# Kernel tuning notes

Hardware: AMD Instinct MI355X
Metric: run time of the kernel (lower is better)

The kernel has to match this reference:

```python
import jax, jax.numpy as jnp
from jax import lax
import numpy as np

SPATIAL_IMPORTANCE = 1.0


def _ssn(x, nspix, n_iter):
    # x: [B, C, H, W]; SLIC-style soft superpixel clustering.
    B, C, H, W = x.shape
    g = int(round(nspix ** 0.5))  # grid side (16 for nspix=256)
    bh, bw = H // g, W // g
    pix = x.reshape(B, C, H * W)                      # [B, C, N]
    # grid initialization of superpixel centers: block-average pooling
    centers = x.reshape(B, C, g, bh, g, bw).mean(axis=(3, 5)).reshape(B, C, nspix)
    p2 = jnp.sum(pix * pix, axis=1)                   # [B, N]

    def affinity(centers):
        c2 = jnp.sum(centers * centers, axis=1)       # [B, K]
        dot = jnp.einsum('bcn,bck->bnk', pix, centers)
        dist = p2[:, :, None] + c2[:, None, :] - 2.0 * dot  # [B, N, K]
        return jax.nn.softmax(-dist, axis=-1)         # soft assignment [B, N, K]

    def step(centers, _):
        aff = affinity(centers)
        wsum = jnp.sum(aff, axis=1)                   # [B, K]
        new_c = jnp.einsum('bcn,bnk->bck', pix, aff) / (wsum[:, None, :] + 1e-16)
        return new_c, None

    centers, _ = lax.scan(step, centers, None, length=n_iter)
    aff = affinity(centers)                           # final soft assignment
    return jnp.transpose(aff, (0, 2, 1))              # [B, K, N]


def setup_inputs() -> dict:
    key = jax.random.key(0)
    x = jax.random.normal(key, (2, 5, 512, 512), dtype=jnp.float32)
    return {"x": x, "nspix": 256, "n_iter": 10}


def reference(x, nspix, n_iter):
    C = x.shape[1]
    scale = jnp.ones((C,), dtype=x.dtype).at[0].set(SPATIAL_IMPORTANCE).at[1].set(SPATIAL_IMPORTANCE)
    x = x * scale[None, :, None, None]
    return _ssn(x, nspix, n_iter)
```

## Files before the change

kernel.cpp:

```cpp
#include <hip/hip_runtime.h>
#include <hip/hip_bf16.h>


#define B_ 2
#define C_ 5
#define H_ 512
#define W_ 512
#define N_ (H_*W_)
#define K_ 256
#define NITER_ 10
#define T_ 512
#define LOG2E 1.4426950408889634f

typedef float f32x8 __attribute__((ext_vector_type(8)));
typedef float f32x4 __attribute__((ext_vector_type(4)));

__global__ __launch_bounds__(256) void init_centers(const float* __restrict__ x,
                                                    float* __restrict__ ctab) {
    int bk  = blockIdx.x;
    int b   = bk >> 8;
    int k   = bk & (K_ - 1);
    int gy  = k >> 4, gx = k & 15;
    int tid = threadIdx.x;

    float s[C_] = {0.f, 0.f, 0.f, 0.f, 0.f};
    for (int i = tid; i < 1024; i += 256) {
        int py = i >> 5, px = i & 31;
        int n  = (gy * 32 + py) * W_ + gx * 32 + px;
        const float* xb = x + (size_t)b * C_ * N_ + n;
        #pragma unroll
        for (int c = 0; c < C_; c++) s[c] += xb[(size_t)c * N_];
    }
    #pragma unroll
    for (int c = 0; c < C_; c++) {
        #pragma unroll
        for (int off = 32; off > 0; off >>= 1)
            s[c] += __shfl_down(s[c], off, 64);
    }
    __shared__ float wred[4][C_];
    int lane = tid & 63, wid = tid >> 6;
    if (lane == 0) {
        #pragma unroll
        for (int c = 0; c < C_; c++) wred[wid][c] = s[c];
    }
    __syncthreads();
    if (tid == 0) {
        float m[C_]; float c2 = 0.f;
        #pragma unroll
        for (int c = 0; c < C_; c++) {
            m[c] = (wred[0][c] + wred[1][c] + wred[2][c] + wred[3][c]) * (1.0f / 1024.0f);
            c2  += m[c] * m[c];
        }
        float* row = ctab + (size_t)(b * K_ + k) * 8;
        #pragma unroll
        for (int c = 0; c < C_; c++) row[c] = 2.0f * LOG2E * m[c];
        row[5] = -LOG2E * c2;
        row[6] = 0.f; row[7] = 0.f;
    }
}

__global__ __launch_bounds__(256, 4) void step_kernel(const float* __restrict__ x,
                                                      const float* __restrict__ ctab,
                                                      float* __restrict__ acc) {
    __shared__ float pl[C_][T_];
    __shared__ float rs[T_];
    int bid = blockIdx.x;
    int b   = bid >> 9;
    int n0  = (bid & 511) * T_;
    int tid = threadIdx.x;

    const float* xb = x + (size_t)b * C_ * N_ + n0;
    #pragma unroll
    for (int c = 0; c < C_; c++) {
        pl[c][tid]       = xb[(size_t)c * N_ + tid];
        pl[c][tid + 256] = xb[(size_t)c * N_ + tid + 256];
    }
    __syncthreads();

    float p0[C_], p1[C_];
    #pragma unroll
    for (int c = 0; c < C_; c++) { p0[c] = pl[c][tid]; p1[c] = pl[c][tid + 256]; }

    const f32x8* crow = (const f32x8*)(ctab + (size_t)b * K_ * 8);
    float S0 = 0.f, S1 = 0.f;
    #pragma unroll 8
    for (int k = 0; k < K_; k++) {
        f32x8 r = crow[k];
        float l0 = r[5], l1 = r[5];
        l0 = fmaf(r[0], p0[0], l0);  l1 = fmaf(r[0], p1[0], l1);
        l0 = fmaf(r[1], p0[1], l0);  l1 = fmaf(r[1], p1[1], l1);
        l0 = fmaf(r[2], p0[2], l0);  l1 = fmaf(r[2], p1[2], l1);
        l0 = fmaf(r[3], p0[3], l0);  l1 = fmaf(r[3], p1[3], l1);
        l0 = fmaf(r[4], p0[4], l0);  l1 = fmaf(r[4], p1[4], l1);
        S0 += __builtin_amdgcn_exp2f(l0);
        S1 += __builtin_amdgcn_exp2f(l1);
    }
    rs[tid]       = 1.0f / S0;
    rs[tid + 256] = 1.0f / S1;
    __syncthreads();

    const float* myrow = ctab + (size_t)(b * K_ + tid) * 8;
    f32x4 r0 = *(const f32x4*)(myrow);
    f32x4 r1 = *(const f32x4*)(myrow + 4);
    float c0 = r0[0], c1 = r0[1], c2v = r0[2], c3 = r0[3], c4 = r1[0], nc2 = r1[1];

    float a0 = 0.f, a1 = 0.f, a2 = 0.f, a3 = 0.f, a4 = 0.f, aw = 0.f;
    #pragma unroll 4
    for (int p = 0; p < T_; p++) {
        float q0 = pl[0][p], q1 = pl[1][p], q2 = pl[2][p];
        float q3 = pl[3][p], q4 = pl[4][p], rr = rs[p];
        float l = nc2;
        l = fmaf(c0, q0, l); l = fmaf(c1, q1, l); l = fmaf(c2v, q2, l);
        l = fmaf(c3, q3, l); l = fmaf(c4, q4, l);
        float af = __builtin_amdgcn_exp2f(l) * rr;
        aw += af;
        a0 = fmaf(q0, af, a0); a1 = fmaf(q1, af, a1); a2 = fmaf(q2, af, a2);
        a3 = fmaf(q3, af, a3); a4 = fmaf(q4, af, a4);
    }
    float* ab = acc + (size_t)b * 6 * K_ + tid;
    unsafeAtomicAdd(ab + 0 * K_, a0);
    unsafeAtomicAdd(ab + 1 * K_, a1);
    unsafeAtomicAdd(ab + 2 * K_, a2);
    unsafeAtomicAdd(ab + 3 * K_, a3);
    unsafeAtomicAdd(ab + 4 * K_, a4);
    unsafeAtomicAdd(ab + 5 * K_, aw);
}

__global__ __launch_bounds__(256) void update_centers(const float* __restrict__ acc,
                                                      float* __restrict__ ctab) {
    int b = blockIdx.x;
    int k = threadIdx.x;
    const float* ab = acc + (size_t)b * 6 * K_ + k;
    float w = ab[5 * K_] + 1e-16f;
    float m[C_]; float c2 = 0.f;
    #pragma unroll
    for (int c = 0; c < C_; c++) { m[c] = ab[(size_t)c * K_] / w; c2 += m[c] * m[c]; }
    float* row = ctab + (size_t)(b * K_ + k) * 8;
    #pragma unroll
    for (int c = 0; c < C_; c++) row[c] = 2.0f * LOG2E * m[c];
    row[5] = -LOG2E * c2;
    row[6] = 0.f; row[7] = 0.f;
}

__global__ __launch_bounds__(256, 4) void final_kernel(const float* __restrict__ x,
                                                       const float* __restrict__ ctab,
                                                       float* __restrict__ out) {
    size_t gid = (size_t)blockIdx.x * 256 + threadIdx.x;
    int b = (int)(gid >> 18);
    int n = (int)(gid & (size_t)(N_ - 1));

    const float* xb = x + (size_t)b * C_ * N_ + n;
    float p[C_];
    #pragma unroll
    for (int c = 0; c < C_; c++) p[c] = xb[(size_t)c * N_];

    const f32x8* crow = (const f32x8*)(ctab + (size_t)b * K_ * 8);
    float S = 0.f;
    #pragma unroll 8
    for (int k = 0; k < K_; k++) {
        f32x8 r = crow[k];
        float l = r[5];
        l = fmaf(r[0], p[0], l); l = fmaf(r[1], p[1], l); l = fmaf(r[2], p[2], l);
        l = fmaf(r[3], p[3], l); l = fmaf(r[4], p[4], l);
        S += __builtin_amdgcn_exp2f(l);
    }
    float rS = 1.0f / S;

    float* ob = out + (size_t)b * K_ * N_ + n;
    #pragma unroll 4
    for (int k = 0; k < K_; k++) {
        f32x8 r = crow[k];
        float l = r[5];
        l = fmaf(r[0], p[0], l); l = fmaf(r[1], p[1], l); l = fmaf(r[2], p[2], l);
        l = fmaf(r[3], p[3], l); l = fmaf(r[4], p[4], l);
        ob[(size_t)k * N_] = __builtin_amdgcn_exp2f(l) * rS;
    }
}

extern "C" void kernel_launch(void* const* d_in, const int* in_sizes, int n_in,
                              void* d_out, int out_size, void* d_ws, size_t ws_size,
                              hipStream_t stream) {
    const float* x = (const float*)d_in[0];
    float* out  = (float*)d_out;
    float* ctab = (float*)d_ws;
    float* acc  = ctab + (size_t)B_ * K_ * 8;

    hipMemsetAsync(acc, 0, (size_t)NITER_ * B_ * 6 * K_ * sizeof(float), stream);

    init_centers<<<B_ * K_, 256, 0, stream>>>(x, ctab);
    for (int s = 0; s < NITER_; s++) {
        float* as = acc + (size_t)s * B_ * 6 * K_;
        step_kernel<<<B_ * (N_ / T_), 256, 0, stream>>>(x, ctab, as);
        update_centers<<<B_, 256, 0, stream>>>(as, ctab);
    }
    final_kernel<<<(B_ * N_) / 256, 256, 0, stream>>>(x, ctab, out);
}
```

Measured before the change: 1.548 ms.

## Register-block four centers per thread and split pixels across waves in step kernel

The accumulation phase of the step kernel is restructured. Each thread now holds four centers in registers and each wave handles a quarter of the tile's pixels, where before every thread walked all 512 pixels for one center. Pixel data is read from LDS as 4-wide vectors and reused across the four centers, which cuts LDS reads per FMA. The per-wave partial sums are then reduced through a shared-memory union before the global atomics. This raises register pressure and adds a cross-wave reduction with extra syncs.

```diff
diff --git a/kernel.cpp b/kernel.cpp
--- a/kernel.cpp
+++ b/kernel.cpp
@@ -62,8 +62,10 @@
 __global__ __launch_bounds__(256, 4) void step_kernel(const float* __restrict__ x,
                                                       const float* __restrict__ ctab,
                                                       float* __restrict__ acc) {
-    __shared__ float pl[C_][T_];
-    __shared__ float rs[T_];
+    __shared__ union SM {
+        struct { float pl[C_][T_]; float rs[T_]; } s;
+        float part[4][6][K_];
+    } sm;
     int bid = blockIdx.x;
     int b   = bid >> 9;
     int n0  = (bid & 511) * T_;
@@ -72,14 +74,14 @@
     const float* xb = x + (size_t)b * C_ * N_ + n0;
     #pragma unroll
     for (int c = 0; c < C_; c++) {
-        pl[c][tid]       = xb[(size_t)c * N_ + tid];
-        pl[c][tid + 256] = xb[(size_t)c * N_ + tid + 256];
-    }
-    __syncthreads();
-
-    float p0[C_], p1[C_];
-    #pragma unroll
-    for (int c = 0; c < C_; c++) { p0[c] = pl[c][tid]; p1[c] = pl[c][tid + 256]; }
+        sm.s.pl[c][tid]       = xb[(size_t)c * N_ + tid];
+        sm.s.pl[c][tid + 256] = xb[(size_t)c * N_ + tid + 256];
+    }
+    __syncthreads();
+
+    float pa[C_], pb[C_];
+    #pragma unroll
+    for (int c = 0; c < C_; c++) { pa[c] = sm.s.pl[c][tid]; pb[c] = sm.s.pl[c][tid + 256]; }
 
     const f32x8* crow = (const f32x8*)(ctab + (size_t)b * K_ * 8);
     float S0 = 0.f, S1 = 0.f;
@@ -87,43 +89,87 @@
     for (int k = 0; k < K_; k++) {
         f32x8 r = crow[k];
         float l0 = r[5], l1 = r[5];
-        l0 = fmaf(r[0], p0[0], l0);  l1 = fmaf(r[0], p1[0], l1);
-        l0 = fmaf(r[1], p0[1], l0);  l1 = fmaf(r[1], p1[1], l1);
-        l0 = fmaf(r[2], p0[2], l0);  l1 = fmaf(r[2], p1[2], l1);
-        l0 = fmaf(r[3], p0[3], l0);  l1 = fmaf(r[3], p1[3], l1);
-        l0 = fmaf(r[4], p0[4], l0);  l1 = fmaf(r[4], p1[4], l1);
+        l0 = fmaf(r[0], pa[0], l0);  l1 = fmaf(r[0], pb[0], l1);
+        l0 = fmaf(r[1], pa[1], l0);  l1 = fmaf(r[1], pb[1], l1);
+        l0 = fmaf(r[2], pa[2], l0);  l1 = fmaf(r[2], pb[2], l1);
+        l0 = fmaf(r[3], pa[3], l0);  l1 = fmaf(r[3], pb[3], l1);
+        l0 = fmaf(r[4], pa[4], l0);  l1 = fmaf(r[4], pb[4], l1);
         S0 += __builtin_amdgcn_exp2f(l0);
         S1 += __builtin_amdgcn_exp2f(l1);
     }
-    rs[tid]       = 1.0f / S0;
-    rs[tid + 256] = 1.0f / S1;
-    __syncthreads();
-
-    const float* myrow = ctab + (size_t)(b * K_ + tid) * 8;
-    f32x4 r0 = *(const f32x4*)(myrow);
-    f32x4 r1 = *(const f32x4*)(myrow + 4);
-    float c0 = r0[0], c1 = r0[1], c2v = r0[2], c3 = r0[3], c4 = r1[0], nc2 = r1[1];
-
-    float a0 = 0.f, a1 = 0.f, a2 = 0.f, a3 = 0.f, a4 = 0.f, aw = 0.f;
-    #pragma unroll 4
-    for (int p = 0; p < T_; p++) {
-        float q0 = pl[0][p], q1 = pl[1][p], q2 = pl[2][p];
-        float q3 = pl[3][p], q4 = pl[4][p], rr = rs[p];
-        float l = nc2;
-        l = fmaf(c0, q0, l); l = fmaf(c1, q1, l); l = fmaf(c2v, q2, l);
-        l = fmaf(c3, q3, l); l = fmaf(c4, q4, l);
-        float af = __builtin_amdgcn_exp2f(l) * rr;
-        aw += af;
-        a0 = fmaf(q0, af, a0); a1 = fmaf(q1, af, a1); a2 = fmaf(q2, af, a2);
-        a3 = fmaf(q3, af, a3); a4 = fmaf(q4, af, a4);
+    sm.s.rs[tid]       = 1.0f / S0;
+    sm.s.rs[tid + 256] = 1.0f / S1;
+    __syncthreads();
+
+    int lane = tid & 63, wid = tid >> 6;
+
+    float cc[4][6];
+    #pragma unroll
+    for (int j = 0; j < 4; j++) {
+        const float* row = ctab + (size_t)(b * K_ + lane + 64 * j) * 8;
+        f32x4 r0 = *(const f32x4*)row;
+        f32x4 r1 = *(const f32x4*)(row + 4);
+        cc[j][0] = r0[0]; cc[j][1] = r0[1]; cc[j][2] = r0[2];
+        cc[j][3] = r0[3]; cc[j][4] = r1[0]; cc[j][5] = r1[1];
+    }
+    float av[4][6];
+    #pragma unroll
+    for (int j = 0; j < 4; j++)
+        #pragma unroll
+        for (int c = 0; c < 6; c++) av[j][c] = 0.f;
+
+    int pbase = wid * 128;
+    #pragma unroll 1
+    for (int p = pbase; p < pbase + 128; p += 4) {
+        f32x4 q0 = *(const f32x4*)&sm.s.pl[0][p];
+        f32x4 q1 = *(const f32x4*)&sm.s.pl[1][p];
+        f32x4 q2 = *(const f32x4*)&sm.s.pl[2][p];
+        f32x4 q3 = *(const f32x4*)&sm.s.pl[3][p];
+        f32x4 q4 = *(const f32x4*)&sm.s.pl[4][p];
+        f32x4 rr = *(const f32x4*)&sm.s.rs[p];
+        #pragma unroll
+        for (int u = 0; u < 4; u++) {
+            #pragma unroll
+            for (int j = 0; j < 4; j++) {
+                float l = cc[j][5];
+                l = fmaf(cc[j][0], q0[u], l);
+                l = fmaf(cc[j][1], q1[u], l);
+                l = fmaf(cc[j][2], q2[u], l);
+                l = fmaf(cc[j][3], q3[u], l);
+                l = fmaf(cc[j][4], q4[u], l);
+                float af = __builtin_amdgcn_exp2f(l) * rr[u];
+                av[j][5] += af;
+                av[j][0] = fmaf(q0[u], af, av[j][0]);
+                av[j][1] = fmaf(q1[u], af, av[j][1]);
+                av[j][2] = fmaf(q2[u], af, av[j][2]);
+                av[j][3] = fmaf(q3[u], af, av[j][3]);
+                av[j][4] = fmaf(q4[u], af, av[j][4]);
+            }
+        }
+    }
+
+    __syncthreads();
+    #pragma unroll
+    for (int j = 0; j < 4; j++)
+        #pragma unroll
+        for (int c = 0; c < 6; c++)
+            sm.part[wid][c][lane + 64 * j] = av[j][c];
+    __syncthreads();
+
+    float s0 = 0.f, s1 = 0.f, s2 = 0.f, s3 = 0.f, s4 = 0.f, sw = 0.f;
+    #pragma unroll
+    for (int w = 0; w < 4; w++) {
+        s0 += sm.part[w][0][tid]; s1 += sm.part[w][1][tid];
+        s2 += sm.part[w][2][tid]; s3 += sm.part[w][3][tid];
+        s4 += sm.part[w][4][tid]; sw += sm.part[w][5][tid];
     }
     float* ab = acc + (size_t)b * 6 * K_ + tid;
-    unsafeAtomicAdd(ab + 0 * K_, a0);
-    unsafeAtomicAdd(ab + 1 * K_, a1);
-    unsafeAtomicAdd(ab + 2 * K_, a2);
-    unsafeAtomicAdd(ab + 3 * K_, a3);
-    unsafeAtomicAdd(ab + 4 * K_, a4);
-    unsafeAtomicAdd(ab + 5 * K_, aw);
+    unsafeAtomicAdd(ab + 0 * K_, s0);
+    unsafeAtomicAdd(ab + 1 * K_, s1);
+    unsafeAtomicAdd(ab + 2 * K_, s2);
+    unsafeAtomicAdd(ab + 3 * K_, s3);
+    unsafeAtomicAdd(ab + 4 * K_, s4);
+    unsafeAtomicAdd(ab + 5 * K_, sw);
 }
 
 __global__ __launch_bounds__(256) void update_centers(const float* __restrict__ acc,
```

Measured after the change: 1.536 ms. About the same (-0.7%).

## Move step kernel distance and center accumulation onto bf16x2-split MFMA

Applied to the files above, without the earlier changes.

The per-iteration step kernel now computes pixel-center logits and the weighted center sums with 16x16x32 bf16 MFMA instead of scalar FMAs. Each fp32 value is split into hi/lo bf16 pairs to keep near-fp32 accuracy. Two prep kernels build the augmented pixel layouts once per call, and a single pass computes exp, row-sum and normalization, replacing the previous two passes over centers. The cost is extra workspace, larger pixel reads, LDS transposes per tile, and lower occupancy.

```diff
diff --git a/kernel.cpp b/kernel.cpp
--- a/kernel.cpp
+++ b/kernel.cpp
@@ -9,14 +9,72 @@
 #define N_ (H_*W_)
 #define K_ 256
 #define NITER_ 10
-#define T_ 512
 #define LOG2E 1.4426950408889634f
 
 typedef float f32x8 __attribute__((ext_vector_type(8)));
 typedef float f32x4 __attribute__((ext_vector_type(4)));
+typedef short bf16x8 __attribute__((ext_vector_type(8)));
+typedef unsigned int u32;
+typedef u32 u32x4 __attribute__((ext_vector_type(4)));
+
+__device__ inline void split2(float a, float b, u32& hi, u32& lo) {
+    u32 ua = __builtin_bit_cast(u32, a), ub = __builtin_bit_cast(u32, b);
+    u32 ha = ua & 0xffff0000u, hb = ub & 0xffff0000u;
+    hi = (ha >> 16) | hb;
+    float la = a - __builtin_bit_cast(float, ha);
+    float lb = b - __builtin_bit_cast(float, hb);
+    lo = (__builtin_bit_cast(u32, la) >> 16) |
+         (__builtin_bit_cast(u32, lb) & 0xffff0000u);
+}
+
+__global__ __launch_bounds__(256) void prep_pix(const float* __restrict__ x,
+                                                u32* __restrict__ pixaug) {
+    size_t i = (size_t)blockIdx.x * 256 + threadIdx.x;
+    int b = (int)(i >> 18);
+    int n = (int)(i & (size_t)(N_ - 1));
+    const float* xb = x + (size_t)b * C_ * N_ + n;
+    float p0 = xb[0], p1 = xb[(size_t)N_], p2 = xb[2*(size_t)N_];
+    float p3 = xb[3*(size_t)N_], p4 = xb[4*(size_t)N_];
+    u32 h01, l01, h23, l23, h45, l45;
+    split2(p0, p1, h01, l01);
+    split2(p2, p3, h23, l23);
+    split2(p4, 1.0f, h45, l45);
+    u32x4* o = (u32x4*)pixaug + (i << 1);
+    o[0] = (u32x4){h01, h23, h45, 0u};
+    o[1] = (u32x4){l01, l23, l45, 0u};
+}
+
+__global__ __launch_bounds__(256) void prep_pixT(const float* __restrict__ x,
+                                                 u32* __restrict__ pixT) {
+    int gi = blockIdx.x * 256 + threadIdx.x;
+    int b = gi >> 15;
+    int g = gi & 32767;
+    const float* xb = x + (size_t)b * C_ * N_ + (size_t)g * 8;
+    u32 hw[8][4], lw[8][4];
+    #pragma unroll
+    for (int c = 0; c < 5; c++) {
+        float pj[8];
+        #pragma unroll
+        for (int j = 0; j < 8; j++) pj[j] = xb[(size_t)c * N_ + j];
+        #pragma unroll
+        for (int w = 0; w < 4; w++) split2(pj[2*w], pj[2*w+1], hw[c][w], lw[c][w]);
+    }
+    #pragma unroll
+    for (int w = 0; w < 4; w++) {
+        hw[5][w] = 0x3F803F80u; lw[5][w] = 0u;
+        hw[6][w] = 0u; lw[6][w] = 0u;
+        hw[7][w] = 0u; lw[7][w] = 0u;
+    }
+    u32x4* o = (u32x4*)pixT + (size_t)gi * 16;
+    #pragma unroll
+    for (int c = 0; c < 8; c++) o[c]     = (u32x4){hw[c][0], hw[c][1], hw[c][2], hw[c][3]};
+    #pragma unroll
+    for (int c = 0; c < 8; c++) o[8 + c] = (u32x4){lw[c][0], lw[c][1], lw[c][2], lw[c][3]};
+}
 
 __global__ __launch_bounds__(256) void init_centers(const float* __restrict__ x,
-                                                    float* __restrict__ ctab) {
+                                                    float* __restrict__ ctab,
+                                                    u32* __restrict__ ctab_bf) {
     int bk  = blockIdx.x;
     int b   = bk >> 8;
     int k   = bk & (K_ - 1);
@@ -51,83 +109,133 @@
             m[c] = (wred[0][c] + wred[1][c] + wred[2][c] + wred[3][c]) * (1.0f / 1024.0f);
             c2  += m[c] * m[c];
         }
+        float r[6];
+        #pragma unroll
+        for (int c = 0; c < C_; c++) r[c] = 2.0f * LOG2E * m[c];
+        r[5] = -LOG2E * c2;
         float* row = ctab + (size_t)(b * K_ + k) * 8;
         #pragma unroll
-        for (int c = 0; c < C_; c++) row[c] = 2.0f * LOG2E * m[c];
-        row[5] = -LOG2E * c2;
+        for (int c = 0; c < 6; c++) row[c] = r[c];
         row[6] = 0.f; row[7] = 0.f;
-    }
-}
-
-__global__ __launch_bounds__(256, 4) void step_kernel(const float* __restrict__ x,
-                                                      const float* __restrict__ ctab,
-                                                      float* __restrict__ acc) {
-    __shared__ float pl[C_][T_];
-    __shared__ float rs[T_];
+        u32 h01, l01, h23, l23, h45, l45;
+        split2(r[0], r[1], h01, l01);
+        split2(r[2], r[3], h23, l23);
+        split2(r[4], r[5], h45, l45);
+        u32x4* cbo = (u32x4*)ctab_bf + (((size_t)(b * K_ + k)) << 1);
+        cbo[0] = (u32x4){h01, h23, h45, 0u};
+        cbo[1] = (u32x4){l01, l23, l45, 0u};
+    }
+}
+
+__global__ __launch_bounds__(256, 2) void step_kernel(
+        const u32* __restrict__ pixaug, const u32* __restrict__ pixT,
+        const u32* __restrict__ ctab_bf, float* __restrict__ acc) {
+    __shared__ u32   tbuf[4][16][20];
+    __shared__ float part[4][6][K_];
+
     int bid = blockIdx.x;
     int b   = bid >> 9;
-    int n0  = (bid & 511) * T_;
+    int n0  = (bid & 511) * 512;
     int tid = threadIdx.x;
-
-    const float* xb = x + (size_t)b * C_ * N_ + n0;
-    #pragma unroll
-    for (int c = 0; c < C_; c++) {
-        pl[c][tid]       = xb[(size_t)c * N_ + tid];
-        pl[c][tid + 256] = xb[(size_t)c * N_ + tid + 256];
+    int lane = tid & 63, wid = tid >> 6;
+    int kc = lane & 15, q = lane >> 4;
+    int selA = q & 1;
+    int selB = q >> 1;
+
+    const u32x4* cbt = (const u32x4*)ctab_bf;
+    const u32x4* pa  = (const u32x4*)pixaug;
+    const u32x4* pt  = (const u32x4*)pixT;
+
+    bf16x8 B1[16];
+    #pragma unroll
+    for (int t = 0; t < 16; t++)
+        B1[t] = __builtin_bit_cast(bf16x8,
+                    cbt[(((size_t)b * K_ + 16 * t + kc) << 1) | (size_t)selB]);
+
+    f32x4 acc2[16];
+    #pragma unroll
+    for (int t = 0; t < 16; t++) acc2[t] = (f32x4){0.f, 0.f, 0.f, 0.f};
+
+    u32* tb = &tbuf[wid][0][0];
+    bool cok = kc < 8;
+    int  cw  = kc & 7;
+
+    for (int s = 0; s < 8; s++) {
+        int p0 = n0 + wid * 128 + 16 * s;
+        bf16x8 A1 = __builtin_bit_cast(bf16x8,
+                        pa[(((size_t)b * N_ + p0 + kc) << 1) | (size_t)selA]);
+        size_t gb = (size_t)b * (N_ >> 3) + (size_t)(p0 >> 3);
+        u32x4 t0 = pt[gb * 16 + (size_t)selA * 8 + cw];
+        u32x4 t1 = pt[(gb + 1) * 16 + (size_t)selA * 8 + cw];
+        if (!cok) { t0 = (u32x4){0,0,0,0}; t1 = (u32x4){0,0,0,0}; }
+        bf16x8 B2h0 = __builtin_bit_cast(bf16x8, t0);
+        bf16x8 B2h1 = __builtin_bit_cast(bf16x8, t1);
+
+        f32x4 P[16];
+        #pragma unroll
+        for (int t = 0; t < 16; t++)
+            P[t] = __builtin_amdgcn_mfma_f32_16x16x32_bf16(
+                       A1, B1[t], (f32x4){0.f, 0.f, 0.f, 0.f}, 0, 0, 0);
+
+        f32x4 S = (f32x4){0.f, 0.f, 0.f, 0.f};
+        #pragma unroll
+        for (int t = 0; t < 16; t++) {
+            #pragma unroll
+            for (int r = 0; r < 4; r++) P[t][r] = __builtin_amdgcn_exp2f(P[t][r]);
+            S += P[t];
+        }
+        #pragma unroll
+        for (int r = 0; r < 4; r++) {
+            float v = S[r];
+            v += __shfl_xor(v, 1); v += __shfl_xor(v, 2);
+            v += __shfl_xor(v, 4); v += __shfl_xor(v, 8);
+            S[r] = 1.0f / v;
+        }
+
+        #pragma unroll
+        for (int t = 0; t < 16; t++) {
+            f32x4 a = P[t] * S;
+            u32 ah01, al01, ah23, al23;
+            split2(a[0], a[1], ah01, al01);
+            split2(a[2], a[3], ah23, al23);
+            *(u32x4*)&tbuf[wid][kc][q * 4] = (u32x4){ah01, ah23, al01, al23};
+            {
+                int wb = kc * 20 + 2 * selB;
+                u32x4 aw = {tb[wb], tb[wb + 1], tb[wb + 4], tb[wb + 5]};
+                bf16x8 A2 = __builtin_bit_cast(bf16x8, aw);
+                acc2[t] = __builtin_amdgcn_mfma_f32_16x16x32_bf16(
+                              A2, B2h0, acc2[t], 0, 0, 0);
+            }
+            {
+                int wb = kc * 20 + 8 + 2 * selB;
+                u32x4 aw = {tb[wb], tb[wb + 1], tb[wb + 4], tb[wb + 5]};
+                bf16x8 A2 = __builtin_bit_cast(bf16x8, aw);
+                acc2[t] = __builtin_amdgcn_mfma_f32_16x16x32_bf16(
+                              A2, B2h1, acc2[t], 0, 0, 0);
+            }
+        }
+    }
+
+    if (kc < 6) {
+        #pragma unroll
+        for (int t = 0; t < 16; t++)
+            #pragma unroll
+            for (int r = 0; r < 4; r++)
+                part[wid][kc][16 * t + 4 * q + r] = acc2[t][r];
     }
     __syncthreads();
-
-    float p0[C_], p1[C_];
-    #pragma unroll
-    for (int c = 0; c < C_; c++) { p0[c] = pl[c][tid]; p1[c] = pl[c][tid + 256]; }
-
-    const f32x8* crow = (const f32x8*)(ctab + (size_t)b * K_ * 8);
-    float S0 = 0.f, S1 = 0.f;
-    #pragma unroll 8
-    for (int k = 0; k < K_; k++) {
-        f32x8 r = crow[k];
-        float l0 = r[5], l1 = r[5];
-        l0 = fmaf(r[0], p0[0], l0);  l1 = fmaf(r[0], p1[0], l1);
-        l0 = fmaf(r[1], p0[1], l0);  l1 = fmaf(r[1], p1[1], l1);
-        l0 = fmaf(r[2], p0[2], l0);  l1 = fmaf(r[2], p1[2], l1);
-        l0 = fmaf(r[3], p0[3], l0);  l1 = fmaf(r[3], p1[3], l1);
-        l0 = fmaf(r[4], p0[4], l0);  l1 = fmaf(r[4], p1[4], l1);
-        S0 += __builtin_amdgcn_exp2f(l0);
-        S1 += __builtin_amdgcn_exp2f(l1);
-    }
-    rs[tid]       = 1.0f / S0;
-    rs[tid + 256] = 1.0f / S1;
-    __syncthreads();
-
-    const float* myrow = ctab + (size_t)(b * K_ + tid) * 8;
-    f32x4 r0 = *(const f32x4*)(myrow);
-    f32x4 r1 = *(const f32x4*)(myrow + 4);
-    float c0 = r0[0], c1 = r0[1], c2v = r0[2], c3 = r0[3], c4 = r1[0], nc2 = r1[1];
-
-    float a0 = 0.f, a1 = 0.f, a2 = 0.f, a3 = 0.f, a4 = 0.f, aw = 0.f;
-    #pragma unroll 4
-    for (int p = 0; p < T_; p++) {
-        float q0 = pl[0][p], q1 = pl[1][p], q2 = pl[2][p];
-        float q3 = pl[3][p], q4 = pl[4][p], rr = rs[p];
-        float l = nc2;
-        l = fmaf(c0, q0, l); l = fmaf(c1, q1, l); l = fmaf(c2v, q2, l);
-        l = fmaf(c3, q3, l); l = fmaf(c4, q4, l);
-        float af = __builtin_amdgcn_exp2f(l) * rr;
-        aw += af;
-        a0 = fmaf(q0, af, a0); a1 = fmaf(q1, af, a1); a2 = fmaf(q2, af, a2);
-        a3 = fmaf(q3, af, a3); a4 = fmaf(q4, af, a4);
-    }
     float* ab = acc + (size_t)b * 6 * K_ + tid;
-    unsafeAtomicAdd(ab + 0 * K_, a0);
-    unsafeAtomicAdd(ab + 1 * K_, a1);
-    unsafeAtomicAdd(ab + 2 * K_, a2);
-    unsafeAtomicAdd(ab + 3 * K_, a3);
-    unsafeAtomicAdd(ab + 4 * K_, a4);
-    unsafeAtomicAdd(ab + 5 * K_, aw);
+    #pragma unroll
+    for (int c = 0; c < 6; c++) {
+        float v = part[0][c][tid] + part[1][c][tid]
+                + part[2][c][tid] + part[3][c][tid];
+        unsafeAtomicAdd(ab + (size_t)c * K_, v);
+    }
 }
 
 __global__ __launch_bounds__(256) void update_centers(const float* __restrict__ acc,
-                                                      float* __restrict__ ctab) {
+                                                      float* __restrict__ ctab,
+                                                      u32* __restrict__ ctab_bf) {
     int b = blockIdx.x;
     int k = threadIdx.x;
     const float* ab = acc + (size_t)b * 6 * K_ + k;
@@ -135,11 +243,21 @@
     float m[C_]; float c2 = 0.f;
     #pragma unroll
     for (int c = 0; c < C_; c++) { m[c] = ab[(size_t)c * K_] / w; c2 += m[c] * m[c]; }
+    float r[6];
+    #pragma unroll
+    for (int c = 0; c < C_; c++) r[c] = 2.0f * LOG2E * m[c];
+    r[5] = -LOG2E * c2;
     float* row = ctab + (size_t)(b * K_ + k) * 8;
     #pragma unroll
-    for (int c = 0; c < C_; c++) row[c] = 2.0f * LOG2E * m[c];
-    row[5] = -LOG2E * c2;
+    for (int c = 0; c < 6; c++) row[c] = r[c];
     row[6] = 0.f; row[7] = 0.f;
+    u32 h01, l01, h23, l23, h45, l45;
+    split2(r[0], r[1], h01, l01);
+    split2(r[2], r[3], h23, l23);
+    split2(r[4], r[5], h45, l45);
+    u32x4* cbo = (u32x4*)ctab_bf + (((size_t)(b * K_ + k)) << 1);
+    cbo[0] = (u32x4){h01, h23, h45, 0u};
+    cbo[1] = (u32x4){l01, l23, l45, 0u};
 }
 
 __global__ __launch_bounds__(256, 4) void final_kernel(const float* __restrict__ x,
@@ -183,15 +301,20 @@
     const float* x = (const float*)d_in[0];
     float* out  = (float*)d_out;
     float* ctab = (float*)d_ws;
-    float* acc  = ctab + (size_t)B_ * K_ * 8;
+    float* acc  = ctab + 4096;
+    u32*  ctab_bf = (u32*)(acc + (size_t)NITER_ * B_ * 6 * K_);
+    u32*  pixaug  = ctab_bf + 4096;
+    u32*  pixT    = pixaug + (size_t)B_ * N_ * 8;
 
     hipMemsetAsync(acc, 0, (size_t)NITER_ * B_ * 6 * K_ * sizeof(float), stream);
 
-    init_centers<<<B_ * K_, 256, 0, stream>>>(x, ctab);
+    prep_pix<<<(B_ * N_) / 256, 256, 0, stream>>>(x, pixaug);
+    prep_pixT<<<(B_ * (N_ / 8)) / 256, 256, 0, stream>>>(x, pixT);
+    init_centers<<<B_ * K_, 256, 0, stream>>>(x, ctab, ctab_bf);
     for (int s = 0; s < NITER_; s++) {
         float* as = acc + (size_t)s * B_ * 6 * K_;
-        step_kernel<<<B_ * (N_ / T_), 256, 0, stream>>>(x, ctab, as);
-        update_centers<<<B_, 256, 0, stream>>>(as, ctab);
+        step_kernel<<<B_ * (N_ / 512), 256, 0, stream>>>(pixaug, pixT, ctab_bf, as);
+        update_centers<<<B_, 256, 0, stream>>>(as, ctab, ctab_bf);
     }
     final_kernel<<<(B_ * N_) / 256, 256, 0, stream>>>(x, ctab, out);
 }
```

Result: faster. 1.357 ms (-12.4%).
